# Kernel tuning notes

Measured on AMD Instinct MI355X. Metric: run time of the kernel, lower is better.

Reference implementation:

```python
import jax, jax.numpy as jnp
import numpy as np


def setup_inputs() -> dict:
    key = jax.random.key(0)
    x = jax.random.normal(key, (8, 256, 16384), dtype=jnp.float32)
    gamma = jnp.zeros((1,), dtype=jnp.float32)
    return {"x": x, "gamma": gamma}


def reference(x, gamma):
    # x: (B, C, T)
    # energy[b, i, j] = sum_t x[b, i, t] * x[b, j, t]  -> (B, C, C)
    energy = jnp.einsum('bit,bjt->bij', x, x)
    # max-subtract trick: attention = softmax(max_j(energy) - energy)
    energy_new = jnp.max(energy, axis=-1, keepdims=True) - energy
    attention = jax.nn.softmax(energy_new, axis=-1)
    # out[b, i, t] = sum_j attention[b, i, j] * x[b, j, t]
    out = jnp.einsum('bij,bjt->bit', attention, x)
    return gamma * out + x
```

## Files before the change

kernel.cpp:

```cpp
#include <hip/hip_runtime.h>
#include <hip/hip_bf16.h>

#define NB 8
#define NC 256
#define NT 16384

using bf16x8 = __attribute__((ext_vector_type(8))) __bf16;
using f32x16 = __attribute__((ext_vector_type(16))) float;
using f32x4  = __attribute__((ext_vector_type(4))) float;
using u32x4  = __attribute__((ext_vector_type(4))) unsigned int;

__device__ __forceinline__ unsigned short bf16_rne(float f) {
  unsigned int u = __float_as_uint(f);
  u += 0x7FFFu + ((u >> 16) & 1u);
  return (unsigned short)(u >> 16);
}

__device__ __forceinline__ unsigned int pack_bf16_pair_rne(float f_lo, float f_hi) {
  unsigned int a = __float_as_uint(f_lo), b = __float_as_uint(f_hi);
  a += 0x7FFFu + ((a >> 16) & 1u);
  b += 0x7FFFu + ((b >> 16) & 1u);
  return __builtin_amdgcn_perm(b, a, 0x07060302u);
}

__device__ __forceinline__ void barrier_acq() {
  __builtin_amdgcn_s_barrier();
  asm volatile("" ::: "memory");
}
__device__ __forceinline__ void barrier_lds_pub() {
  asm volatile("s_waitcnt lgkmcnt(0)" ::: "memory");
  __builtin_amdgcn_s_barrier();
  asm volatile("" ::: "memory");
}

template <int ITERS>
__global__ __launch_bounds__(1024) void k_gram(const float* __restrict__ x,
                                               float* __restrict__ Gp) {
  __shared__ __align__(16) unsigned short lds[256 * 72];
  const int b   = blockIdx.y;
  const int kc  = blockIdx.x;
  const int tid = threadIdx.x;
  const int l   = tid & 63, w = tid >> 6;
  const int wr  = w >> 2, wc = w & 3;
  const int l31 = l & 31, lh = l >> 5;

  const float* __restrict__ xb = x + (size_t)b * NC * NT;

  const int sr = tid >> 2;
  const int sq = tid & 3;
  const float* sp = xb + (size_t)sr * NT + kc * (ITERS * 64) + sq * 16;

  f32x4 r0 = ((const f32x4*)sp)[0];
  f32x4 r1 = ((const f32x4*)sp)[1];
  f32x4 r2 = ((const f32x4*)sp)[2];
  f32x4 r3 = ((const f32x4*)sp)[3];

  f32x16 acc00, acc01, acc10, acc11;
#pragma unroll
  for (int i = 0; i < 16; ++i) { acc00[i] = 0.f; acc01[i] = 0.f; acc10[i] = 0.f; acc11[i] = 0.f; }

#pragma unroll 1
  for (int it = 0; it < ITERS; ++it) {
    barrier_acq();
    u32x4 p0, p1;
    p0[0] = pack_bf16_pair_rne(r0[0], r0[1]); p0[1] = pack_bf16_pair_rne(r0[2], r0[3]);
    p0[2] = pack_bf16_pair_rne(r1[0], r1[1]); p0[3] = pack_bf16_pair_rne(r1[2], r1[3]);
    p1[0] = pack_bf16_pair_rne(r2[0], r2[1]); p1[1] = pack_bf16_pair_rne(r2[2], r2[3]);
    p1[2] = pack_bf16_pair_rne(r3[0], r3[1]); p1[3] = pack_bf16_pair_rne(r3[2], r3[3]);
    u32x4* dst = (u32x4*)&lds[sr * 72 + sq * 16];
    dst[0] = p0;
    dst[1] = p1;
    if (it < ITERS - 1) {
      const float* np = sp + (it + 1) * 64;
      r0 = ((const f32x4*)np)[0]; r1 = ((const f32x4*)np)[1];
      r2 = ((const f32x4*)np)[2]; r3 = ((const f32x4*)np)[3];
    }
    barrier_lds_pub();
#pragma unroll
    for (int s = 0; s < 4; ++s) {
      const int ko = s * 16 + lh * 8;
      bf16x8 a0 = *(const bf16x8*)&lds[(wr * 64 +      l31) * 72 + ko];
      bf16x8 a1 = *(const bf16x8*)&lds[(wr * 64 + 32 + l31) * 72 + ko];
      bf16x8 b0 = *(const bf16x8*)&lds[(wc * 64 +      l31) * 72 + ko];
      bf16x8 b1 = *(const bf16x8*)&lds[(wc * 64 + 32 + l31) * 72 + ko];
      acc00 = __builtin_amdgcn_mfma_f32_32x32x16_bf16(a0, b0, acc00, 0, 0, 0);
      acc01 = __builtin_amdgcn_mfma_f32_32x32x16_bf16(a0, b1, acc01, 0, 0, 0);
      acc10 = __builtin_amdgcn_mfma_f32_32x32x16_bf16(a1, b0, acc10, 0, 0, 0);
      acc11 = __builtin_amdgcn_mfma_f32_32x32x16_bf16(a1, b1, acc11, 0, 0, 0);
    }
  }

  float* __restrict__ Gb = Gp + ((size_t)kc * NB + b) * NC * NC;
  const int ibase = wr * 64 + 4 * lh;
  const int jbase = wc * 64 + l31;
#pragma unroll
  for (int g = 0; g < 16; ++g) {
    const int ir = (g & 3) + 8 * (g >> 2);
    Gb[(ibase + ir) * NC      + jbase     ] = acc00[g];
    Gb[(ibase + ir) * NC      + jbase + 32] = acc01[g];
    Gb[(ibase + 32 + ir) * NC + jbase     ] = acc10[g];
    Gb[(ibase + 32 + ir) * NC + jbase + 32] = acc11[g];
  }
}

template <int NKC>
__global__ __launch_bounds__(256) void k_softmax(const float* __restrict__ Gp,
                                                 const float* __restrict__ gamma,
                                                 unsigned short* __restrict__ Att) {
  const int row = blockIdx.x * 4 + (threadIdx.x >> 6);
  const int l   = threadIdx.x & 63;
  const int i   = row & (NC - 1);
  const float* base = Gp + (size_t)row * NC + l * 4;

  f32x4 v; v[0] = 0.f; v[1] = 0.f; v[2] = 0.f; v[3] = 0.f;
#pragma unroll
  for (int kc = 0; kc < NKC; ++kc) {
    f32x4 p = *(const f32x4*)(base + (size_t)kc * (NB * NC * NC));
    v[0] += p[0]; v[1] += p[1]; v[2] += p[2]; v[3] += p[3];
  }

  float mn = fminf(fminf(v[0], v[1]), fminf(v[2], v[3]));
#pragma unroll
  for (int m = 32; m >= 1; m >>= 1) mn = fminf(mn, __shfl_xor(mn, m, 64));
  float p0 = __expf(mn - v[0]), p1 = __expf(mn - v[1]);
  float p2 = __expf(mn - v[2]), p3 = __expf(mn - v[3]);
  float s = (p0 + p1) + (p2 + p3);
#pragma unroll
  for (int m = 32; m >= 1; m >>= 1) s += __shfl_xor(s, m, 64);
  const float sc = gamma[0] / s;

  const int j0 = 4 * l;
  ushort4 o;
  o.x = bf16_rne(p0 * sc + ((j0 + 0) == i ? 1.f : 0.f));
  o.y = bf16_rne(p1 * sc + ((j0 + 1) == i ? 1.f : 0.f));
  o.z = bf16_rne(p2 * sc + ((j0 + 2) == i ? 1.f : 0.f));
  o.w = bf16_rne(p3 * sc + ((j0 + 3) == i ? 1.f : 0.f));
  *(ushort4*)(Att + (size_t)row * NC + j0) = o;
}

__global__ __launch_bounds__(1024) void k_out(const float* __restrict__ x,
                                              const unsigned short* __restrict__ Att,
                                              float* __restrict__ y) {
  __shared__ __align__(16) float bs[32 * 260];
  __shared__ __align__(16) unsigned short as_[256 * 40];
  const int b   = blockIdx.y;
  const int t0  = blockIdx.x * 256;
  const int tid = threadIdx.x;
  const int l   = tid & 63, w = tid >> 6;
  const int rbw = w >> 3, cbw = w & 7;
  const int l31 = l & 31, lh = l >> 5;

  const float* __restrict__ xb = x + (size_t)b * NC * NT;
  const unsigned short* __restrict__ Ab = Att + (size_t)b * NC * NC;

  const int bk = tid >> 5, bf = tid & 31;
  const int ar = tid >> 2, aseg = tid & 3;

  const float* bsp = xb + (size_t)bk * NT + t0 + bf * 4;
  f32x4 rb0 = *(const f32x4*)bsp;
  f32x4 rb1 = *(const f32x4*)(bsp + 128);
  u32x4 ra  = *(const u32x4*)(Ab + ar * NC + aseg * 8);

  f32x16 acc0, acc1, acc2, acc3;
#pragma unroll
  for (int i = 0; i < 16; ++i) { acc0[i] = 0.f; acc1[i] = 0.f; acc2[i] = 0.f; acc3[i] = 0.f; }

#pragma unroll 1
  for (int it = 0; it < 8; ++it) {
    barrier_acq();
    *(f32x4*)&bs[bk * 260 + bf * 4]       = rb0;
    *(f32x4*)&bs[bk * 260 + 128 + bf * 4] = rb1;
    *(u32x4*)&as_[ar * 40 + aseg * 8]     = ra;
    if (it < 7) {
      const float* np = bsp + (size_t)(it + 1) * 32 * NT;
      rb0 = *(const f32x4*)np;
      rb1 = *(const f32x4*)(np + 128);
      ra  = *(const u32x4*)(Ab + ar * NC + (it + 1) * 32 + aseg * 8);
    }
    barrier_lds_pub();
#pragma unroll
    for (int s = 0; s < 2; ++s) {
      const int kr = s * 16 + lh * 8;
      const int tc = cbw * 32 + l31;
      float f0 = bs[(kr + 0) * 260 + tc], f1 = bs[(kr + 1) * 260 + tc];
      float f2 = bs[(kr + 2) * 260 + tc], f3 = bs[(kr + 3) * 260 + tc];
      float f4 = bs[(kr + 4) * 260 + tc], f5 = bs[(kr + 5) * 260 + tc];
      float f6 = bs[(kr + 6) * 260 + tc], f7 = bs[(kr + 7) * 260 + tc];
      u32x4 pk;
      pk[0] = pack_bf16_pair_rne(f0, f1); pk[1] = pack_bf16_pair_rne(f2, f3);
      pk[2] = pack_bf16_pair_rne(f4, f5); pk[3] = pack_bf16_pair_rne(f6, f7);
      bf16x8 bfrag = __builtin_bit_cast(bf16x8, pk);
      const int ao = s * 16 + lh * 8;
      bf16x8 a0 = *(const bf16x8*)&as_[(rbw * 128 +      l31) * 40 + ao];
      bf16x8 a1 = *(const bf16x8*)&as_[(rbw * 128 + 32 + l31) * 40 + ao];
      bf16x8 a2 = *(const bf16x8*)&as_[(rbw * 128 + 64 + l31) * 40 + ao];
      bf16x8 a3 = *(const bf16x8*)&as_[(rbw * 128 + 96 + l31) * 40 + ao];
      acc0 = __builtin_amdgcn_mfma_f32_32x32x16_bf16(a0, bfrag, acc0, 0, 0, 0);
      acc1 = __builtin_amdgcn_mfma_f32_32x32x16_bf16(a1, bfrag, acc1, 0, 0, 0);
      acc2 = __builtin_amdgcn_mfma_f32_32x32x16_bf16(a2, bfrag, acc2, 0, 0, 0);
      acc3 = __builtin_amdgcn_mfma_f32_32x32x16_bf16(a3, bfrag, acc3, 0, 0, 0);
    }
  }

  const int tg = t0 + cbw * 32 + l31;
  const int ib = rbw * 128 + 4 * lh;
#pragma unroll
  for (int g = 0; g < 16; ++g) {
    const int ir = (g & 3) + 8 * (g >> 2);
    size_t i0 = (size_t)(b * NC + ib + ir) * NT + tg;
    __builtin_nontemporal_store(acc0[g], &y[i0]);
    __builtin_nontemporal_store(acc1[g], &y[i0 + (size_t)32 * NT]);
    __builtin_nontemporal_store(acc2[g], &y[i0 + (size_t)64 * NT]);
    __builtin_nontemporal_store(acc3[g], &y[i0 + (size_t)96 * NT]);
  }
}

extern "C" void kernel_launch(void* const* d_in, const int* in_sizes, int n_in,
                              void* d_out, int out_size, void* d_ws, size_t ws_size,
                              hipStream_t stream) {
  const float* x     = (const float*)d_in[0];
  const float* gamma = (const float*)d_in[1];
  float* y = (float*)d_out;

  const size_t chunk_bytes = (size_t)NB * NC * NC * sizeof(float);
  const size_t att_bytes   = (size_t)NB * NC * NC * sizeof(unsigned short);

  int nkc;
  if      (ws_size >= 32 * chunk_bytes + att_bytes) nkc = 32;
  else if (ws_size >= 16 * chunk_bytes + att_bytes) nkc = 16;
  else if (ws_size >=  8 * chunk_bytes + att_bytes) nkc = 8;
  else                                              nkc = 4;

  float* Gp = (float*)d_ws;
  unsigned short* Att = (unsigned short*)((char*)d_ws + (size_t)nkc * chunk_bytes);

  switch (nkc) {
    case 32:
      k_gram<8>  <<<dim3(32, NB), 1024, 0, stream>>>(x, Gp);
      k_softmax<32><<<dim3(NB * NC / 4), 256, 0, stream>>>(Gp, gamma, Att);
      break;
    case 16:
      k_gram<16> <<<dim3(16, NB), 1024, 0, stream>>>(x, Gp);
      k_softmax<16><<<dim3(NB * NC / 4), 256, 0, stream>>>(Gp, gamma, Att);
      break;
    case 8:
      k_gram<32> <<<dim3(8, NB), 1024, 0, stream>>>(x, Gp);
      k_softmax<8><<<dim3(NB * NC / 4), 256, 0, stream>>>(Gp, gamma, Att);
      break;
    default:
      k_gram<64> <<<dim3(4, NB), 1024, 0, stream>>>(x, Gp);
      k_softmax<4><<<dim3(NB * NC / 4), 256, 0, stream>>>(Gp, gamma, Att);
      break;
  }
  k_out<<<dim3(NT / 256, NB), 1024, 0, stream>>>(x, Att, y);
}
```

Before: 274.7 us.

## Double-buffer LDS in gram and output kernels to drop one barrier per iteration

Both the gram kernel and the output kernel now use two LDS buffers. Each iteration writes the next tile into the alternate buffer while MFMAs read the current one, and the pre-write barrier is removed, leaving one barrier per iteration instead of two. Global prefetch now runs two iterations ahead. The cost is doubled shared-memory use in both kernels, which with 1024-thread blocks may limit occupancy, plus slightly more register pressure.

Result: no change. 278.5 us (+1.4%).

```diff
diff --git a/kernel.cpp b/kernel.cpp
--- a/kernel.cpp
+++ b/kernel.cpp
@@ -23,10 +23,6 @@
   return __builtin_amdgcn_perm(b, a, 0x07060302u);
 }
 
-__device__ __forceinline__ void barrier_acq() {
-  __builtin_amdgcn_s_barrier();
-  asm volatile("" ::: "memory");
-}
 __device__ __forceinline__ void barrier_lds_pub() {
   asm volatile("s_waitcnt lgkmcnt(0)" ::: "memory");
   __builtin_amdgcn_s_barrier();
@@ -36,7 +32,7 @@
 template <int ITERS>
 __global__ __launch_bounds__(1024) void k_gram(const float* __restrict__ x,
                                                float* __restrict__ Gp) {
-  __shared__ __align__(16) unsigned short lds[256 * 72];
+  __shared__ __align__(16) unsigned short lds[2][256 * 72];
   const int b   = blockIdx.y;
   const int kc  = blockIdx.x;
   const int tid = threadIdx.x;
@@ -49,45 +45,62 @@
   const int sr = tid >> 2;
   const int sq = tid & 3;
   const float* sp = xb + (size_t)sr * NT + kc * (ITERS * 64) + sq * 16;
+  const int soff = sr * 72 + sq * 16;
 
   f32x4 r0 = ((const f32x4*)sp)[0];
   f32x4 r1 = ((const f32x4*)sp)[1];
   f32x4 r2 = ((const f32x4*)sp)[2];
   f32x4 r3 = ((const f32x4*)sp)[3];
-
-  f32x16 acc00, acc01, acc10, acc11;
-#pragma unroll
-  for (int i = 0; i < 16; ++i) { acc00[i] = 0.f; acc01[i] = 0.f; acc10[i] = 0.f; acc11[i] = 0.f; }
-
-#pragma unroll 1
-  for (int it = 0; it < ITERS; ++it) {
-    barrier_acq();
+  {
     u32x4 p0, p1;
     p0[0] = pack_bf16_pair_rne(r0[0], r0[1]); p0[1] = pack_bf16_pair_rne(r0[2], r0[3]);
     p0[2] = pack_bf16_pair_rne(r1[0], r1[1]); p0[3] = pack_bf16_pair_rne(r1[2], r1[3]);
     p1[0] = pack_bf16_pair_rne(r2[0], r2[1]); p1[1] = pack_bf16_pair_rne(r2[2], r2[3]);
     p1[2] = pack_bf16_pair_rne(r3[0], r3[1]); p1[3] = pack_bf16_pair_rne(r3[2], r3[3]);
-    u32x4* dst = (u32x4*)&lds[sr * 72 + sq * 16];
-    dst[0] = p0;
-    dst[1] = p1;
+    u32x4* dst = (u32x4*)&lds[0][soff];
+    dst[0] = p0; dst[1] = p1;
+  }
+  if (ITERS > 1) {
+    const float* np = sp + 64;
+    r0 = ((const f32x4*)np)[0]; r1 = ((const f32x4*)np)[1];
+    r2 = ((const f32x4*)np)[2]; r3 = ((const f32x4*)np)[3];
+  }
+  barrier_lds_pub();
+
+  f32x16 acc00, acc01, acc10, acc11;
+#pragma unroll
+  for (int i = 0; i < 16; ++i) { acc00[i] = 0.f; acc01[i] = 0.f; acc10[i] = 0.f; acc11[i] = 0.f; }
+
+#pragma unroll 1
+  for (int it = 0; it < ITERS; ++it) {
     if (it < ITERS - 1) {
-      const float* np = sp + (it + 1) * 64;
+      u32x4 p0, p1;
+      p0[0] = pack_bf16_pair_rne(r0[0], r0[1]); p0[1] = pack_bf16_pair_rne(r0[2], r0[3]);
+      p0[2] = pack_bf16_pair_rne(r1[0], r1[1]); p0[3] = pack_bf16_pair_rne(r1[2], r1[3]);
+      p1[0] = pack_bf16_pair_rne(r2[0], r2[1]); p1[1] = pack_bf16_pair_rne(r2[2], r2[3]);
+      p1[2] = pack_bf16_pair_rne(r3[0], r3[1]); p1[3] = pack_bf16_pair_rne(r3[2], r3[3]);
+      u32x4* dst = (u32x4*)&lds[(it + 1) & 1][soff];
+      dst[0] = p0; dst[1] = p1;
+    }
+    if (it < ITERS - 2) {
+      const float* np = sp + (it + 2) * 64;
       r0 = ((const f32x4*)np)[0]; r1 = ((const f32x4*)np)[1];
       r2 = ((const f32x4*)np)[2]; r3 = ((const f32x4*)np)[3];
     }
-    barrier_lds_pub();
+    const unsigned short* cur = lds[it & 1];
 #pragma unroll
     for (int s = 0; s < 4; ++s) {
       const int ko = s * 16 + lh * 8;
-      bf16x8 a0 = *(const bf16x8*)&lds[(wr * 64 +      l31) * 72 + ko];
-      bf16x8 a1 = *(const bf16x8*)&lds[(wr * 64 + 32 + l31) * 72 + ko];
-      bf16x8 b0 = *(const bf16x8*)&lds[(wc * 64 +      l31) * 72 + ko];
-      bf16x8 b1 = *(const bf16x8*)&lds[(wc * 64 + 32 + l31) * 72 + ko];
+      bf16x8 a0 = *(const bf16x8*)&cur[(wr * 64 +      l31) * 72 + ko];
+      bf16x8 a1 = *(const bf16x8*)&cur[(wr * 64 + 32 + l31) * 72 + ko];
+      bf16x8 b0 = *(const bf16x8*)&cur[(wc * 64 +      l31) * 72 + ko];
+      bf16x8 b1 = *(const bf16x8*)&cur[(wc * 64 + 32 + l31) * 72 + ko];
       acc00 = __builtin_amdgcn_mfma_f32_32x32x16_bf16(a0, b0, acc00, 0, 0, 0);
       acc01 = __builtin_amdgcn_mfma_f32_32x32x16_bf16(a0, b1, acc01, 0, 0, 0);
       acc10 = __builtin_amdgcn_mfma_f32_32x32x16_bf16(a1, b0, acc10, 0, 0, 0);
       acc11 = __builtin_amdgcn_mfma_f32_32x32x16_bf16(a1, b1, acc11, 0, 0, 0);
     }
+    barrier_lds_pub();
   }
 
   float* __restrict__ Gb = Gp + ((size_t)kc * NB + b) * NC * NC;
@@ -141,8 +154,8 @@
 __global__ __launch_bounds__(1024) void k_out(const float* __restrict__ x,
                                               const unsigned short* __restrict__ Att,
                                               float* __restrict__ y) {
-  __shared__ __align__(16) float bs[32 * 260];
-  __shared__ __align__(16) unsigned short as_[256 * 40];
+  __shared__ __align__(16) float bs[2][32 * 260];
+  __shared__ __align__(16) unsigned short as_[2][256 * 40];
   const int b   = blockIdx.y;
   const int t0  = blockIdx.x * 256;
   const int tid = threadIdx.x;
@@ -157,9 +170,22 @@
   const int ar = tid >> 2, aseg = tid & 3;
 
   const float* bsp = xb + (size_t)bk * NT + t0 + bf * 4;
+  const int boff = bk * 260 + bf * 4;
+  const int aoff = ar * 40 + aseg * 8;
+
   f32x4 rb0 = *(const f32x4*)bsp;
   f32x4 rb1 = *(const f32x4*)(bsp + 128);
   u32x4 ra  = *(const u32x4*)(Ab + ar * NC + aseg * 8);
+  *(f32x4*)&bs[0][boff]       = rb0;
+  *(f32x4*)&bs[0][boff + 128] = rb1;
+  *(u32x4*)&as_[0][aoff]      = ra;
+  {
+    const float* np = bsp + (size_t)32 * NT;
+    rb0 = *(const f32x4*)np;
+    rb1 = *(const f32x4*)(np + 128);
+    ra  = *(const u32x4*)(Ab + ar * NC + 32 + aseg * 8);
+  }
+  barrier_lds_pub();
 
   f32x16 acc0, acc1, acc2, acc3;
 #pragma unroll
@@ -167,39 +193,43 @@
 
 #pragma unroll 1
   for (int it = 0; it < 8; ++it) {
-    barrier_acq();
-    *(f32x4*)&bs[bk * 260 + bf * 4]       = rb0;
-    *(f32x4*)&bs[bk * 260 + 128 + bf * 4] = rb1;
-    *(u32x4*)&as_[ar * 40 + aseg * 8]     = ra;
     if (it < 7) {
-      const float* np = bsp + (size_t)(it + 1) * 32 * NT;
+      const int nb = (it + 1) & 1;
+      *(f32x4*)&bs[nb][boff]       = rb0;
+      *(f32x4*)&bs[nb][boff + 128] = rb1;
+      *(u32x4*)&as_[nb][aoff]      = ra;
+    }
+    if (it < 6) {
+      const float* np = bsp + (size_t)(it + 2) * 32 * NT;
       rb0 = *(const f32x4*)np;
       rb1 = *(const f32x4*)(np + 128);
-      ra  = *(const u32x4*)(Ab + ar * NC + (it + 1) * 32 + aseg * 8);
-    }
-    barrier_lds_pub();
+      ra  = *(const u32x4*)(Ab + ar * NC + (it + 2) * 32 + aseg * 8);
+    }
+    const float* bcur = bs[it & 1];
+    const unsigned short* acur = as_[it & 1];
 #pragma unroll
     for (int s = 0; s < 2; ++s) {
       const int kr = s * 16 + lh * 8;
       const int tc = cbw * 32 + l31;
-      float f0 = bs[(kr + 0) * 260 + tc], f1 = bs[(kr + 1) * 260 + tc];
-      float f2 = bs[(kr + 2) * 260 + tc], f3 = bs[(kr + 3) * 260 + tc];
-      float f4 = bs[(kr + 4) * 260 + tc], f5 = bs[(kr + 5) * 260 + tc];
-      float f6 = bs[(kr + 6) * 260 + tc], f7 = bs[(kr + 7) * 260 + tc];
+      float f0 = bcur[(kr + 0) * 260 + tc], f1 = bcur[(kr + 1) * 260 + tc];
+      float f2 = bcur[(kr + 2) * 260 + tc], f3 = bcur[(kr + 3) * 260 + tc];
+      float f4 = bcur[(kr + 4) * 260 + tc], f5 = bcur[(kr + 5) * 260 + tc];
+      float f6 = bcur[(kr + 6) * 260 + tc], f7 = bcur[(kr + 7) * 260 + tc];
       u32x4 pk;
       pk[0] = pack_bf16_pair_rne(f0, f1); pk[1] = pack_bf16_pair_rne(f2, f3);
       pk[2] = pack_bf16_pair_rne(f4, f5); pk[3] = pack_bf16_pair_rne(f6, f7);
       bf16x8 bfrag = __builtin_bit_cast(bf16x8, pk);
       const int ao = s * 16 + lh * 8;
-      bf16x8 a0 = *(const bf16x8*)&as_[(rbw * 128 +      l31) * 40 + ao];
-      bf16x8 a1 = *(const bf16x8*)&as_[(rbw * 128 + 32 + l31) * 40 + ao];
-      bf16x8 a2 = *(const bf16x8*)&as_[(rbw * 128 + 64 + l31) * 40 + ao];
-      bf16x8 a3 = *(const bf16x8*)&as_[(rbw * 128 + 96 + l31) * 40 + ao];
+      bf16x8 a0 = *(const bf16x8*)&acur[(rbw * 128 +      l31) * 40 + ao];
+      bf16x8 a1 = *(const bf16x8*)&acur[(rbw * 128 + 32 + l31) * 40 + ao];
+      bf16x8 a2 = *(const bf16x8*)&acur[(rbw * 128 + 64 + l31) * 40 + ao];
+      bf16x8 a3 = *(const bf16x8*)&acur[(rbw * 128 + 96 + l31) * 40 + ao];
       acc0 = __builtin_amdgcn_mfma_f32_32x32x16_bf16(a0, bfrag, acc0, 0, 0, 0);
       acc1 = __builtin_amdgcn_mfma_f32_32x32x16_bf16(a1, bfrag, acc1, 0, 0, 0);
       acc2 = __builtin_amdgcn_mfma_f32_32x32x16_bf16(a2, bfrag, acc2, 0, 0, 0);
       acc3 = __builtin_amdgcn_mfma_f32_32x32x16_bf16(a3, bfrag, acc3, 0, 0, 0);
     }
+    barrier_lds_pub();
   }
 
   const int tg = t0 + cbw * 32 + l31;
```
